# Kernel tuning notes

Hardware: AMD Instinct MI355X
Metric: run time of the kernel (lower is better)

Reference implementation:

```python
import jax, jax.numpy as jnp
import numpy as np

S, TM1, B, V, E, H = 96, 96, 8, 32000, 256, 512
PAD = 0
NEG = -1e30


def setup_inputs() -> dict:
    key = jax.random.key(0)
    ks = jax.random.split(key, 10)
    n = lambda k, shape, s=0.05: (jax.random.normal(k, shape, jnp.float32) * s)
    return {
        "src": jax.random.randint(ks[0], (S, B), 0, V, jnp.int32),
        "tgt": jax.random.randint(ks[1], (TM1 + 1, B), 0, V, jnp.int32),
        "emb": n(ks[2], (V, E)),
        "W_ih": n(ks[3], (4 * H, E)),
        "W_hh": n(ks[4], (4 * H, H)),
        "b_ih": jnp.zeros((4 * H,), jnp.float32),
        "b_hh": jnp.zeros((4 * H,), jnp.float32),
        "W_att": n(ks[5], (H, H)),
        "sent": n(ks[6], (H,)),
        "W_read": n(ks[7], (V, H)),
    }


def _lstm_cell(x, h, c, W_ih, W_hh, b_ih, b_hh):
    g = x @ W_ih.T + b_ih + h @ W_hh.T + b_hh
    i, f, gg, o = jnp.split(g, 4, axis=-1)
    c = jax.nn.sigmoid(f) * c + jax.nn.sigmoid(i) * jnp.tanh(gg)
    h = jax.nn.sigmoid(o) * jnp.tanh(c)
    return h, c


def _forward(src, tgt, emb, W_ih, W_hh, b_ih, b_hh, W_att, sent, W_read):
    # padding_idx behavior: pad row of embedding is zero (and gets no grad)
    emb_eff = emb * (jnp.arange(V) != PAD).astype(emb.dtype)[:, None]
    xs = jnp.concatenate([emb_eff[src], emb_eff[tgt[:-1]]], axis=0)  # [S+TM1,B,E]

    def step(carry, x):
        h, c = carry
        h, c = _lstm_cell(x, h, c, W_ih, W_hh, b_ih, b_hh)
        return (h, c), h

    init = (jnp.zeros((B, H), xs.dtype), jnp.zeros((B, H), xs.dtype))
    _, H_all = jax.lax.scan(step, init, xs)  # [S+TM1,B,H]

    H_dec = H_all[S:]                              # [TM1,B,H]
    Q = jnp.tanh(H_dec @ W_att.T)                  # [TM1,B,H]
    Z = jnp.einsum("tbh,jbh->tjb", Q, H_all)      # [TM1,S+TM1,B]
    zs = jnp.einsum("tbh,h->tb", Q, sent)         # sentinel logit
    logits = jnp.concatenate([Z, zs[:, None, :]], axis=1)  # [TM1,S+TM1+1,B]

    j = jnp.arange(S + TM1 + 1)
    t = jnp.arange(TM1)
    valid = (j[None, :] < S + t[:, None] + 1) | (j[None, :] == S + TM1)
    logits = jnp.where(valid[:, :, None], logits, NEG)
    a = jax.nn.softmax(logits, axis=1)
    a_src, a_tgt, a_sent = a[:, :S], a[:, S:S + TM1], a[:, -1]

    # pointer distributions via scatter-add (avoids dense one-hot [S,B,V])
    b_idx = jnp.arange(B)[None, None, :]
    t_idx = jnp.arange(TM1)[:, None, None]
    p_ptr = jnp.zeros((TM1, B, V), a.dtype)
    p_ptr = p_ptr.at[t_idx, b_idx, src[None, :, :]].add(a_src)
    p_ptr = p_ptr.at[t_idx, b_idx, tgt[:-1][None, :, :]].add(a_tgt)

    p_vocab = jax.nn.softmax(H_dec @ W_read.T, axis=-1)  # [TM1,B,V]
    p = p_ptr + p_vocab * a_sent[:, :, None]
    ptr_scores = p_ptr + a_sent[:, :, None]

    mask = (tgt != PAD).astype(p.dtype)  # [TM1+1,B]
    gold = jnp.take_along_axis(jnp.log(p), tgt[1:][:, :, None], axis=2)[..., 0] * mask[1:]
    gold_ptr = jnp.take_along_axis(jnp.log(ptr_scores), tgt[1:][:, :, None], axis=2)[..., 0] * mask[1:]
    return gold.sum(0), gold_ptr.sum(0)  # ([B], [B])


def reference(src, tgt, emb, W_ih, W_hh, b_ih, b_hh, W_att, sent, W_read):
    return _forward(src, tgt, emb, W_ih, W_hh, b_ih, b_hh, W_att, sent, W_read)
```

## Files before the change

### kernel.cpp

```cpp
#include <hip/hip_runtime.h>
#include <math.h>

#define SS   96
#define TM   96
#define BB   8
#define VV   32000
#define EE   256
#define HH   512
#define NTOK (SS + TM)
#define G4   (4 * HH)
#define NEGF (-1e30f)
#define LBLK 16
#define NVT  (VV / 64)

#define NXIH  768
#define NCVTW 512
#define NCVTR 8000
#define NPREP (NXIH + NCVTW + NCVTR)

typedef __attribute__((ext_vector_type(8))) short short8;
typedef __attribute__((ext_vector_type(4))) float f32x4;
typedef __attribute__((ext_vector_type(4))) unsigned uint32x4;
typedef unsigned long long u64;

#define XIH_OFF   ((size_t)0)
#define XIH_SZ    ((size_t)NTOK * BB * G4)
#define HALL_OFF  (XIH_OFF + XIH_SZ)
#define HALL_SZ   ((size_t)NTOK * BB * HH)
#define Q_OFF     (HALL_OFF + HALL_SZ)
#define Q_SZ      ((size_t)TM * BB * HH)
#define PPTR_OFF  (Q_OFF + Q_SZ)
#define ASENT_OFF (PPTR_OFF + (size_t)(TM * BB))
#define SSUM_OFF  (ASENT_OFF + (size_t)(TM * BB))
#define LSTAR_OFF (SSUM_OFF + (size_t)(TM * BB))
#define FLAG_OFF  (LSTAR_OFF + (size_t)(TM * BB))
#define HBF_OFF   (FLAG_OFF + (size_t)1024)
#define HBF_SZF   ((size_t)2 * BB * HH / 2)
#define WHHBF_OFF (HBF_OFF + HBF_SZF)
#define WHHBF_SZF ((size_t)G4 * HH / 2)
#define ABF_OFF   (WHHBF_OFF + WHHBF_SZF)
#define ABF_SZF   ((size_t)(TM * BB) * HH / 2)
#define WBF_OFF   (ABF_OFF + ABF_SZF)
#define WBF_SZF   ((size_t)VV * HH / 2)
#define PSUM_OFF  (WBF_OFF + WBF_SZF)
#define PSUM_SZF  ((size_t)NVT * (TM * BB))
#define NEED_F    (PSUM_OFF + PSUM_SZF)

__device__ __forceinline__ float sigf(float x) { return 1.f / (1.f + __expf(-x)); }

__device__ __forceinline__ unsigned short f2bf(float x) {
    unsigned bits = __float_as_uint(x);
    bits += 0x7FFFu + ((bits >> 16) & 1u);
    return (unsigned short)(bits >> 16);
}

__global__ void __launch_bounds__(256) k_prep(const int* __restrict__ src,
                                              const int* __restrict__ tgt,
                                              const float* __restrict__ emb,
                                              const float* __restrict__ Wih,
                                              const float* __restrict__ bih,
                                              const float* __restrict__ bhh,
                                              const float* __restrict__ Whh,
                                              const float* __restrict__ Wread,
                                              float* __restrict__ xih,
                                              unsigned short* __restrict__ whhbf,
                                              unsigned short* __restrict__ wbf) {
    __shared__ float xs[16 * EE];
    const int bid = blockIdx.x;
    const int tid = threadIdx.x;

    if (bid < NXIH) {
        const int tok0 = (bid >> 3) * 16;
        const int row0 = (bid & 7) * 256;
        for (int e = tid; e < 16 * EE; e += 256) {
            int tk = e >> 8, k = e & 255;
            int tau = tok0 + tk;
            int idx = (tau < SS * BB) ? src[tau] : tgt[tau - SS * BB];
            xs[tk * EE + k] = (idx == 0) ? 0.f : emb[(size_t)idx * EE + k];
        }
        __syncthreads();

        const int row = row0 + tid;
        const float bias = bih[row] + bhh[row];
        float acc[16];
#pragma unroll
        for (int r = 0; r < 16; ++r) acc[r] = bias;
        const float4* w4 = (const float4*)(Wih + (size_t)row * EE);
        for (int k4 = 0; k4 < EE / 4; ++k4) {
            float4 w = w4[k4];
#pragma unroll
            for (int r = 0; r < 16; ++r) {
                float4 x = *((const float4*)&xs[r * EE + k4 * 4]);
                acc[r] += w.x * x.x + w.y * x.y + w.z * x.z + w.w * x.w;
            }
        }
#pragma unroll
        for (int r = 0; r < 16; ++r)
            xih[(size_t)(tok0 + r) * G4 + row] = acc[r];
        return;
    }

    const float* srcp;
    unsigned short* dstp;
    size_t base;
    if (bid < NXIH + NCVTW) { srcp = Whh;   dstp = whhbf; base = (size_t)(bid - NXIH) * 2048; }
    else                    { srcp = Wread; dstp = wbf;   base = (size_t)(bid - NXIH - NCVTW) * 2048; }
    base += (size_t)tid * 8;
    float4 f0 = *(const float4*)(srcp + base);
    float4 f1 = *(const float4*)(srcp + base + 4);
    uint4 o;
    o.x = (unsigned)f2bf(f0.x) | ((unsigned)f2bf(f0.y) << 16);
    o.y = (unsigned)f2bf(f0.z) | ((unsigned)f2bf(f0.w) << 16);
    o.z = (unsigned)f2bf(f1.x) | ((unsigned)f2bf(f1.y) << 16);
    o.w = (unsigned)f2bf(f1.z) | ((unsigned)f2bf(f1.w) << 16);
    *(uint4*)(dstp + base) = o;
}

__global__ void __launch_bounds__(256, 1) k_lstm(const float* __restrict__ xih,
                                                 const unsigned short* __restrict__ whhbf,
                                                 float* __restrict__ hall,
                                                 unsigned short* __restrict__ hbf,
                                                 unsigned short* __restrict__ abf,
                                                 unsigned* __restrict__ flags) {
    __shared__ short lA[65536];
    const int tid = threadIdx.x;
    const int wv  = tid >> 6;
    const int l   = tid & 63;
    const int b16 = l & 15;
    const int kg  = l >> 4;
    const int bb  = b16 & 7;
    const int bx  = blockIdx.x;
    const int I0  = bx * 32 + wv * 8;

    const int j = b16;
    const unsigned short* a0p = whhbf + ((size_t)((j >> 3) * HH + I0 + (j & 7))) * HH + kg * 8;
    const unsigned short* a1p = whhbf + ((size_t)((2 + (j >> 3)) * HH + I0 + (j & 7))) * HH + kg * 8;
    short* lA0 = lA + (((size_t)wv * 2 + 0) * 16 * 64 + l) * 8;
    short* lA1 = lA + (((size_t)wv * 2 + 1) * 16 * 64 + l) * 8;
#pragma unroll
    for (int ks = 0; ks < 16; ++ks) {
        *(short8*)(lA0 + ks * 512) = *(const short8*)(a0p + ks * 32);
        *(short8*)(lA1 + ks * 512) = *(const short8*)(a1p + ks * 32);
    }
    __syncthreads();

    const int xgate0 = (kg >> 1);
    const int xgate1 = 2 + (kg >> 1);
    const int xi     = I0 + (kg & 1) * 4;

    float c0[4] = {0.f, 0.f, 0.f, 0.f};
    union fragu { uint32x4 u4; short8 s; };

    for (int t = 0; t < NTOK; ++t) {
        const float* xb = xih + ((size_t)t * BB + bb) * G4;
        float4 x0 = *(const float4*)(xb + xgate0 * HH + xi);
        float4 x1 = *(const float4*)(xb + xgate1 * HH + xi);

        fragu Bf[16];
        if (t > 0) {
            if (l < 16) {
                while (__hip_atomic_load(&flags[(size_t)l * 16], __ATOMIC_RELAXED,
                                         __HIP_MEMORY_SCOPE_AGENT) < (unsigned)t) {}
            }
            const unsigned short* hsrc =
                hbf + ((t - 1) & 1) * (BB * HH) + (size_t)bb * HH + kg * 8;
#pragma unroll
            for (int ks = 0; ks < 16; ++ks)
                asm volatile("global_load_dwordx4 %0, %1, off sc0 sc1"
                             : "=v"(Bf[ks].u4) : "v"(hsrc + ks * 32) : "memory");
            asm volatile("s_waitcnt vmcnt(0)" ::: "memory");
            __builtin_amdgcn_sched_barrier(0);
        }

        f32x4 acc0 = {x0.x, x0.y, x0.z, x0.w};
        f32x4 acc1 = {x1.x, x1.y, x1.z, x1.w};
        if (t > 0) {
#pragma unroll
            for (int ks = 0; ks < 16; ++ks) {
                short8 a0 = *(const short8*)(lA0 + ks * 512);
                short8 a1 = *(const short8*)(lA1 + ks * 512);
                acc0 = __builtin_amdgcn_mfma_f32_16x16x32_bf16(a0, Bf[ks].s, acc0, 0, 0, 0);
                acc1 = __builtin_amdgcn_mfma_f32_16x16x32_bf16(a1, Bf[ks].s, acc1, 0, 0, 0);
            }
        }

        float hreg[4];
#pragma unroll
        for (int r = 0; r < 4; ++r) {
            float gf = __shfl_down(acc0[r], 32, 64);
            float go = __shfl_down(acc1[r], 32, 64);
            float is = sigf(acc0[r]);
            float fs = sigf(gf);
            float gv = tanhf(acc1[r]);
            float os = sigf(go);
            c0[r] = fs * c0[r] + is * gv;
            hreg[r] = os * tanhf(c0[r]);
        }

        if (l < 32 && b16 < BB) {
            const int ib = I0 + kg * 4;
            *(float4*)(hall + ((size_t)t * BB + b16) * HH + ib) =
                make_float4(hreg[0], hreg[1], hreg[2], hreg[3]);
            u64 pk = (u64)f2bf(hreg[0]) | ((u64)f2bf(hreg[1]) << 16) |
                     ((u64)f2bf(hreg[2]) << 32) | ((u64)f2bf(hreg[3]) << 48);
            if (t >= SS)
                *(u64*)(abf + ((size_t)(t - SS) * BB + b16) * HH + ib) = pk;
            if (t < NTOK - 1) {
                unsigned short* hdst = hbf + (t & 1) * (BB * HH) + (size_t)b16 * HH + ib;
                asm volatile("global_store_dwordx2 %0, %1, off sc0 sc1"
                             :: "v"(hdst), "v"(pk) : "memory");
            }
        }

        if (t < NTOK - 1) {
            asm volatile("s_waitcnt vmcnt(0)" ::: "memory");
            __syncthreads();
            if (tid == 0)
                __hip_atomic_store(&flags[(size_t)bx * 16], (unsigned)(t + 1),
                                   __ATOMIC_RELAXED, __HIP_MEMORY_SCOPE_AGENT);
        }
    }
}

__global__ void __launch_bounds__(256) k_q(const float* __restrict__ hall,
                                           const float* __restrict__ Watt,
                                           float* __restrict__ q) {
    __shared__ float hb[8 * 516];
    const int t = blockIdx.x, tid = threadIdx.x;
    const float* hdec = hall + (size_t)(SS + t) * (BB * HH);
    for (int e = tid; e < BB * HH; e += 256)
        hb[(e >> 9) * 516 + (e & 511)] = hdec[e];
    __syncthreads();

    for (int oi = tid; oi < BB * HH; oi += 256) {
        int b = oi & 7, ii = oi >> 3;
        const float4* w4 = (const float4*)(Watt + (size_t)ii * HH);
        const float4* h4 = (const float4*)(hb + b * 516);
        float acc = 0.f;
        for (int k4 = 0; k4 < HH / 4; ++k4) {
            float4 w = w4[k4], h = h4[k4];
            acc += w.x * h.x + w.y * h.y + w.z * h.z + w.w * h.w;
        }
        q[(size_t)(t * BB + b) * HH + ii] = tanhf(acc);
    }
}

__global__ void __launch_bounds__(256) k_att(const float* __restrict__ hall,
                                             const float* __restrict__ q,
                                             const float* __restrict__ sent,
                                             const int* __restrict__ src,
                                             const int* __restrict__ tgt,
                                             float* __restrict__ pptr,
                                             float* __restrict__ asent) {
    __shared__ float qs[HH];
    __shared__ float av[256];
    __shared__ float red[256];
    const int t = blockIdx.x, b = blockIdx.y, tid = threadIdx.x;

    for (int e = tid; e < HH; e += 256) qs[e] = q[(size_t)(t * BB + b) * HH + e];
    __syncthreads();

    const int j = tid;
    float acc = NEGF;
    if (j < SS + TM + 1) {
        bool valid = (j < SS + t + 1) || (j == SS + TM);
        if (valid) {
            const float* vptr = (j < SS + TM) ? (hall + (size_t)(j * BB + b) * HH) : sent;
            const float4* v4 = (const float4*)vptr;
            const float4* q4 = (const float4*)qs;
            float a = 0.f;
            for (int k4 = 0; k4 < HH / 4; ++k4) {
                float4 v = v4[k4], qq = q4[k4];
                a += v.x * qq.x + v.y * qq.y + v.z * qq.z + v.w * qq.w;
            }
            acc = a;
        }
    }
    red[tid] = acc;
    __syncthreads();
    for (int s2 = 128; s2 > 0; s2 >>= 1) {
        if (tid < s2) red[tid] = fmaxf(red[tid], red[tid + s2]);
        __syncthreads();
    }
    float m = red[0];
    __syncthreads();
    float e = __expf(acc - m);
    red[tid] = e;
    __syncthreads();
    for (int s2 = 128; s2 > 0; s2 >>= 1) {
        if (tid < s2) red[tid] += red[tid + s2];
        __syncthreads();
    }
    float denom = red[0];
    __syncthreads();
    float a = e / denom;
    av[tid] = a;
    __syncthreads();

    const int vs = tgt[(t + 1) * BB + b];
    float contrib = 0.f;
    if (j < SS) {
        if (src[j * BB + b] == vs) contrib += av[j];
        if (tgt[j * BB + b] == vs) contrib += av[SS + j];
    }
    red[tid] = contrib;
    __syncthreads();
    for (int s2 = 128; s2 > 0; s2 >>= 1) {
        if (tid < s2) red[tid] += red[tid + s2];
        __syncthreads();
    }
    if (tid == 0) {
        pptr[t * BB + b]  = red[0];
        asent[t * BB + b] = av[SS + TM];
    }
}

__global__ void __launch_bounds__(256) k_vocab_mfma(const unsigned short* __restrict__ Abf,
                                                    const unsigned short* __restrict__ Wbf,
                                                    const int* __restrict__ tgt,
                                                    float* __restrict__ psum,
                                                    float* __restrict__ lstar) {
    __shared__ short lB[32768];
    const int tid  = threadIdx.x;
    const int lane = tid & 63;
    const int r16  = lane & 15;
    const int kg   = lane >> 4;
    const int n0   = blockIdx.x * 64;

    for (int s = tid; s < 4096; s += 256) {
        const int slot = s >> 6;
        const int cb = slot >> 4, ks = slot & 15;
        const int ll = s & 63;
        const int rr = ll & 15, kk = ll >> 4;
        *(short8*)(lB + (size_t)s * 8) =
            *(const short8*)(Wbf + (size_t)(n0 + cb * 16 + rr) * HH + ks * 32 + kk * 8);
    }
    __syncthreads();

    const short* lBme = lB + (size_t)lane * 8;

    for (int pass = 0; pass < 12; ++pass) {
        const int row0 = pass * 64 + (tid >> 6) * 16;
        const unsigned short* arow = Abf + (size_t)(row0 + r16) * HH + kg * 8;

        f32x4 acc0 = {0.f,0.f,0.f,0.f}, acc1 = acc0, acc2 = acc0, acc3 = acc0;
#pragma unroll
        for (int ks = 0; ks < 16; ++ks) {
            short8 a = *(const short8*)(arow + ks * 32);
            acc0 = __builtin_amdgcn_mfma_f32_16x16x32_bf16(a, *(const short8*)(lBme + (size_t)(0 * 16 + ks) * 512), acc0, 0, 0, 0);
            acc1 = __builtin_amdgcn_mfma_f32_16x16x32_bf16(a, *(const short8*)(lBme + (size_t)(1 * 16 + ks) * 512), acc1, 0, 0, 0);
            acc2 = __builtin_amdgcn_mfma_f32_16x16x32_bf16(a, *(const short8*)(lBme + (size_t)(2 * 16 + ks) * 512), acc2, 0, 0, 0);
            acc3 = __builtin_amdgcn_mfma_f32_16x16x32_bf16(a, *(const short8*)(lBme + (size_t)(3 * 16 + ks) * 512), acc3, 0, 0, 0);
        }

#pragma unroll
        for (int reg = 0; reg < 4; ++reg) {
            const int rowg = row0 + 4 * kg + reg;
            const int vs = tgt[BB + rowg];
            int cg;
            cg = n0 +  0 + r16; if (cg == vs) lstar[rowg] = acc0[reg];
            cg = n0 + 16 + r16; if (cg == vs) lstar[rowg] = acc1[reg];
            cg = n0 + 32 + r16; if (cg == vs) lstar[rowg] = acc2[reg];
            cg = n0 + 48 + r16; if (cg == vs) lstar[rowg] = acc3[reg];

            float v = __expf(acc0[reg]) + __expf(acc1[reg]) +
                      __expf(acc2[reg]) + __expf(acc3[reg]);
            v += __shfl_xor(v, 1, 64);
            v += __shfl_xor(v, 2, 64);
            v += __shfl_xor(v, 4, 64);
            v += __shfl_xor(v, 8, 64);
            if (r16 == 0) psum[(size_t)blockIdx.x * (TM * BB) + rowg] = v;
        }
    }
}

__global__ void __launch_bounds__(256) k_vocab_f32(const float* __restrict__ hall,
                                                   const float* __restrict__ Wread,
                                                   const int* __restrict__ tgt,
                                                   float* __restrict__ ssum,
                                                   float* __restrict__ lstar) {
    __shared__ float hs[32 * HH];
    const int tid = threadIdx.x;
    const int v0 = blockIdx.x * 512 + tid * 2;
    const int v1 = v0 + 1;
    const bool g0 = v0 < VV, g1 = v1 < VV;
    const float4* w40 = (const float4*)(Wread + (size_t)(g0 ? v0 : 0) * HH);
    const float4* w41 = (const float4*)(Wread + (size_t)(g1 ? v1 : 0) * HH);
    const int rbase0 = blockIdx.y * 128;

    for (int ch = 0; ch < 4; ++ch) {
        const int rbase = rbase0 + ch * 32;
        const float4* sp4 = (const float4*)(hall + ((size_t)SS * BB + rbase) * HH);
        float4* hs4 = (float4*)hs;
        for (int e = tid; e < 32 * HH / 4; e += 256) hs4[e] = sp4[e];
        __syncthreads();

        float acc0[32], acc1[32];
#pragma unroll
        for (int r = 0; r < 32; ++r) { acc0[r] = 0.f; acc1[r] = 0.f; }

        for (int k4 = 0; k4 < HH / 4; ++k4) {
            float4 w0 = w40[k4];
            float4 w1 = w41[k4];
#pragma unroll
            for (int r = 0; r < 32; ++r) {
                float4 h = *((const float4*)(hs + r * HH + k4 * 4));
                acc0[r] += w0.x * h.x + w0.y * h.y + w0.z * h.z + w0.w * h.w;
                acc1[r] += w1.x * h.x + w1.y * h.y + w1.z * h.z + w1.w * h.w;
            }
        }

#pragma unroll
        for (int r = 0; r < 32; ++r) {
            const int row = rbase + r;
            float val = 0.f;
            if (g0) val += __expf(acc0[r]);
            if (g1) val += __expf(acc1[r]);
#pragma unroll
            for (int d = 32; d > 0; d >>= 1) val += __shfl_xor(val, d, 64);
            if ((tid & 63) == 0) atomicAdd(&ssum[row], val);
            const int vs = tgt[row + BB];
            if (g0 && v0 == vs) lstar[row] = acc0[r];
            else if (g1 && v1 == vs) lstar[row] = acc1[r];
        }
        __syncthreads();
    }
}

__global__ void __launch_bounds__(768) k_final(const float* __restrict__ pptr,
                                               const float* __restrict__ asent,
                                               const float* __restrict__ ssum,
                                               const float* __restrict__ lstar,
                                               const float* __restrict__ psum,
                                               const int use_psum,
                                               const int* __restrict__ tgt,
                                               float* __restrict__ out) {
    __shared__ float g[TM * BB], gp[TM * BB];
    const int tid = threadIdx.x;
    float ss;
    if (use_psum) {
        float s0 = 0.f, s1 = 0.f, s2 = 0.f, s3 = 0.f;
        for (int q = 0; q < NVT; q += 4) {
            s0 += psum[(size_t)(q + 0) * (TM * BB) + tid];
            s1 += psum[(size_t)(q + 1) * (TM * BB) + tid];
            s2 += psum[(size_t)(q + 2) * (TM * BB) + tid];
            s3 += psum[(size_t)(q + 3) * (TM * BB) + tid];
        }
        ss = (s0 + s1) + (s2 + s3);
    } else {
        ss = ssum[tid];
    }

    const int vs = tgt[tid + BB];
    const float pv = __expf(lstar[tid]) / ss;
    const float ps = pptr[tid];
    const float as = asent[tid];
    if (vs != 0) {
        g[tid]  = logf(ps + pv * as);
        gp[tid] = logf(ps + as);
    } else {
        g[tid] = 0.f; gp[tid] = 0.f;
    }
    __syncthreads();
    if (tid < BB) {
        float su1 = 0.f, su2 = 0.f;
        for (int t = 0; t < TM; ++t) { su1 += g[t * BB + tid]; su2 += gp[t * BB + tid]; }
        out[tid] = su1;
        out[BB + tid] = su2;
    }
}

extern "C" void kernel_launch(void* const* d_in, const int* in_sizes, int n_in,
                              void* d_out, int out_size, void* d_ws, size_t ws_size,
                              hipStream_t stream) {
    (void)in_sizes; (void)n_in; (void)out_size;
    const int*   src   = (const int*)d_in[0];
    const int*   tgt   = (const int*)d_in[1];
    const float* emb   = (const float*)d_in[2];
    const float* Wih   = (const float*)d_in[3];
    const float* Whh   = (const float*)d_in[4];
    const float* bih   = (const float*)d_in[5];
    const float* bhh   = (const float*)d_in[6];
    const float* Watt  = (const float*)d_in[7];
    const float* sent  = (const float*)d_in[8];
    const float* Wread = (const float*)d_in[9];
    float* ws  = (float*)d_ws;
    float* out = (float*)d_out;

    const bool use_mfma_vocab = ws_size >= NEED_F * sizeof(float);

    (void)hipMemsetAsync((void*)(ws + SSUM_OFF), 0, (size_t)2560 * sizeof(float), stream);

    k_prep<<<dim3(NPREP), 256, 0, stream>>>(
        src, tgt, emb, Wih, bih, bhh, Whh, Wread,
        ws + XIH_OFF, (unsigned short*)(ws + WHHBF_OFF), (unsigned short*)(ws + WBF_OFF));

    k_lstm<<<dim3(LBLK), 256, 0, stream>>>(
        ws + XIH_OFF, (const unsigned short*)(ws + WHHBF_OFF), ws + HALL_OFF,
        (unsigned short*)(ws + HBF_OFF), (unsigned short*)(ws + ABF_OFF),
        (unsigned*)(ws + FLAG_OFF));

    k_q<<<dim3(TM), 256, 0, stream>>>(ws + HALL_OFF, Watt, ws + Q_OFF);

    k_att<<<dim3(TM, BB), 256, 0, stream>>>(ws + HALL_OFF, ws + Q_OFF, sent,
                                            src, tgt, ws + PPTR_OFF, ws + ASENT_OFF);

    if (use_mfma_vocab) {
        k_vocab_mfma<<<dim3(NVT), 256, 0, stream>>>(
            (const unsigned short*)(ws + ABF_OFF),
            (const unsigned short*)(ws + WBF_OFF),
            tgt, ws + PSUM_OFF, ws + LSTAR_OFF);
    } else {
        k_vocab_f32<<<dim3(63, 6), 256, 0, stream>>>(ws + HALL_OFF, Wread, tgt,
                                                     ws + SSUM_OFF, ws + LSTAR_OFF);
    }

    k_final<<<dim3(1), dim3(TM * BB), 0, stream>>>(ws + PPTR_OFF, ws + ASENT_OFF,
                                                   ws + SSUM_OFF, ws + LSTAR_OFF,
                                                   ws + PSUM_OFF, use_mfma_vocab ? 1 : 0,
                                                   tgt, out);
}
```

Baseline: 1.237 ms.

## Fuse bf16 weight conversion into consumers and merge attention with vocab kernel

```diff
diff --git a/kernel.cpp b/kernel.cpp
--- a/kernel.cpp
+++ b/kernel.cpp
@@ -12,11 +12,7 @@
 #define NEGF (-1e30f)
 #define LBLK 16
 #define NVT  (VV / 64)
-
-#define NXIH  768
-#define NCVTW 512
-#define NCVTR 8000
-#define NPREP (NXIH + NCVTW + NCVTR)
+#define NXIH 768
 
 typedef __attribute__((ext_vector_type(8))) short short8;
 typedef __attribute__((ext_vector_type(4))) float f32x4;
@@ -36,13 +32,9 @@
 #define FLAG_OFF  (LSTAR_OFF + (size_t)(TM * BB))
 #define HBF_OFF   (FLAG_OFF + (size_t)1024)
 #define HBF_SZF   ((size_t)2 * BB * HH / 2)
-#define WHHBF_OFF (HBF_OFF + HBF_SZF)
-#define WHHBF_SZF ((size_t)G4 * HH / 2)
-#define ABF_OFF   (WHHBF_OFF + WHHBF_SZF)
+#define ABF_OFF   (HBF_OFF + HBF_SZF)
 #define ABF_SZF   ((size_t)(TM * BB) * HH / 2)
-#define WBF_OFF   (ABF_OFF + ABF_SZF)
-#define WBF_SZF   ((size_t)VV * HH / 2)
-#define PSUM_OFF  (WBF_OFF + WBF_SZF)
+#define PSUM_OFF  (ABF_OFF + ABF_SZF)
 #define PSUM_SZF  ((size_t)NVT * (TM * BB))
 #define NEED_F    (PSUM_OFF + PSUM_SZF)
 
@@ -52,6 +44,13 @@
     unsigned bits = __float_as_uint(x);
     bits += 0x7FFFu + ((bits >> 16) & 1u);
     return (unsigned short)(bits >> 16);
+}
+
+__device__ __forceinline__ short8 pack_bf8(float4 f0, float4 f1) {
+    union { unsigned short u[8]; short8 s; } r;
+    r.u[0] = f2bf(f0.x); r.u[1] = f2bf(f0.y); r.u[2] = f2bf(f0.z); r.u[3] = f2bf(f0.w);
+    r.u[4] = f2bf(f1.x); r.u[5] = f2bf(f1.y); r.u[6] = f2bf(f1.z); r.u[7] = f2bf(f1.w);
+    return r.s;
 }
 
 __global__ void __launch_bounds__(256) k_prep(const int* __restrict__ src,
@@ -60,64 +59,42 @@
                                               const float* __restrict__ Wih,
                                               const float* __restrict__ bih,
                                               const float* __restrict__ bhh,
-                                              const float* __restrict__ Whh,
-                                              const float* __restrict__ Wread,
-                                              float* __restrict__ xih,
-                                              unsigned short* __restrict__ whhbf,
-                                              unsigned short* __restrict__ wbf) {
+                                              float* __restrict__ xih) {
     __shared__ float xs[16 * EE];
     const int bid = blockIdx.x;
     const int tid = threadIdx.x;
 
-    if (bid < NXIH) {
-        const int tok0 = (bid >> 3) * 16;
-        const int row0 = (bid & 7) * 256;
-        for (int e = tid; e < 16 * EE; e += 256) {
-            int tk = e >> 8, k = e & 255;
-            int tau = tok0 + tk;
-            int idx = (tau < SS * BB) ? src[tau] : tgt[tau - SS * BB];
-            xs[tk * EE + k] = (idx == 0) ? 0.f : emb[(size_t)idx * EE + k];
-        }
-        __syncthreads();
-
-        const int row = row0 + tid;
-        const float bias = bih[row] + bhh[row];
-        float acc[16];
-#pragma unroll
-        for (int r = 0; r < 16; ++r) acc[r] = bias;
-        const float4* w4 = (const float4*)(Wih + (size_t)row * EE);
-        for (int k4 = 0; k4 < EE / 4; ++k4) {
-            float4 w = w4[k4];
-#pragma unroll
-            for (int r = 0; r < 16; ++r) {
-                float4 x = *((const float4*)&xs[r * EE + k4 * 4]);
-                acc[r] += w.x * x.x + w.y * x.y + w.z * x.z + w.w * x.w;
-            }
-        }
-#pragma unroll
-        for (int r = 0; r < 16; ++r)
-            xih[(size_t)(tok0 + r) * G4 + row] = acc[r];
-        return;
-    }
-
-    const float* srcp;
-    unsigned short* dstp;
-    size_t base;
-    if (bid < NXIH + NCVTW) { srcp = Whh;   dstp = whhbf; base = (size_t)(bid - NXIH) * 2048; }
-    else                    { srcp = Wread; dstp = wbf;   base = (size_t)(bid - NXIH - NCVTW) * 2048; }
-    base += (size_t)tid * 8;
-    float4 f0 = *(const float4*)(srcp + base);
-    float4 f1 = *(const float4*)(srcp + base + 4);
-    uint4 o;
-    o.x = (unsigned)f2bf(f0.x) | ((unsigned)f2bf(f0.y) << 16);
-    o.y = (unsigned)f2bf(f0.z) | ((unsigned)f2bf(f0.w) << 16);
-    o.z = (unsigned)f2bf(f1.x) | ((unsigned)f2bf(f1.y) << 16);
-    o.w = (unsigned)f2bf(f1.z) | ((unsigned)f2bf(f1.w) << 16);
-    *(uint4*)(dstp + base) = o;
+    const int tok0 = (bid >> 3) * 16;
+    const int row0 = (bid & 7) * 256;
+    for (int e = tid; e < 16 * EE; e += 256) {
+        int tk = e >> 8, k = e & 255;
+        int tau = tok0 + tk;
+        int idx = (tau < SS * BB) ? src[tau] : tgt[tau - SS * BB];
+        xs[tk * EE + k] = (idx == 0) ? 0.f : emb[(size_t)idx * EE + k];
+    }
+    __syncthreads();
+
+    const int row = row0 + tid;
+    const float bias = bih[row] + bhh[row];
+    float acc[16];
+#pragma unroll
+    for (int r = 0; r < 16; ++r) acc[r] = bias;
+    const float4* w4 = (const float4*)(Wih + (size_t)row * EE);
+    for (int k4 = 0; k4 < EE / 4; ++k4) {
+        float4 w = w4[k4];
+#pragma unroll
+        for (int r = 0; r < 16; ++r) {
+            float4 x = *((const float4*)&xs[r * EE + k4 * 4]);
+            acc[r] += w.x * x.x + w.y * x.y + w.z * x.z + w.w * x.w;
+        }
+    }
+#pragma unroll
+    for (int r = 0; r < 16; ++r)
+        xih[(size_t)(tok0 + r) * G4 + row] = acc[r];
 }
 
 __global__ void __launch_bounds__(256, 1) k_lstm(const float* __restrict__ xih,
-                                                 const unsigned short* __restrict__ whhbf,
+                                                 const float* __restrict__ Whh,
                                                  float* __restrict__ hall,
                                                  unsigned short* __restrict__ hbf,
                                                  unsigned short* __restrict__ abf,
@@ -133,14 +110,16 @@
     const int I0  = bx * 32 + wv * 8;
 
     const int j = b16;
-    const unsigned short* a0p = whhbf + ((size_t)((j >> 3) * HH + I0 + (j & 7))) * HH + kg * 8;
-    const unsigned short* a1p = whhbf + ((size_t)((2 + (j >> 3)) * HH + I0 + (j & 7))) * HH + kg * 8;
+    const float* a0f = Whh + ((size_t)((j >> 3) * HH + I0 + (j & 7))) * HH + kg * 8;
+    const float* a1f = Whh + ((size_t)((2 + (j >> 3)) * HH + I0 + (j & 7))) * HH + kg * 8;
     short* lA0 = lA + (((size_t)wv * 2 + 0) * 16 * 64 + l) * 8;
     short* lA1 = lA + (((size_t)wv * 2 + 1) * 16 * 64 + l) * 8;
 #pragma unroll
     for (int ks = 0; ks < 16; ++ks) {
-        *(short8*)(lA0 + ks * 512) = *(const short8*)(a0p + ks * 32);
-        *(short8*)(lA1 + ks * 512) = *(const short8*)(a1p + ks * 32);
+        *(short8*)(lA0 + ks * 512) =
+            pack_bf8(*(const float4*)(a0f + ks * 32), *(const float4*)(a0f + ks * 32 + 4));
+        *(short8*)(lA1 + ks * 512) =
+            pack_bf8(*(const float4*)(a1f + ks * 32), *(const float4*)(a1f + ks * 32 + 4));
     }
     __syncthreads();
 
@@ -245,18 +224,15 @@
     }
 }
 
-__global__ void __launch_bounds__(256) k_att(const float* __restrict__ hall,
-                                             const float* __restrict__ q,
-                                             const float* __restrict__ sent,
-                                             const int* __restrict__ src,
-                                             const int* __restrict__ tgt,
-                                             float* __restrict__ pptr,
-                                             float* __restrict__ asent) {
-    __shared__ float qs[HH];
-    __shared__ float av[256];
-    __shared__ float red[256];
-    const int t = blockIdx.x, b = blockIdx.y, tid = threadIdx.x;
-
+__device__ __forceinline__ void att_body(int t, int b, int tid,
+                                         const float* __restrict__ hall,
+                                         const float* __restrict__ q,
+                                         const float* __restrict__ sent,
+                                         const int* __restrict__ src,
+                                         const int* __restrict__ tgt,
+                                         float* __restrict__ pptr,
+                                         float* __restrict__ asent,
+                                         float* qs, float* av, float* red) {
     for (int e = tid; e < HH; e += 256) qs[e] = q[(size_t)(t * BB + b) * HH + e];
     __syncthreads();
 
@@ -315,25 +291,58 @@
     }
 }
 
-__global__ void __launch_bounds__(256) k_vocab_mfma(const unsigned short* __restrict__ Abf,
-                                                    const unsigned short* __restrict__ Wbf,
-                                                    const int* __restrict__ tgt,
-                                                    float* __restrict__ psum,
-                                                    float* __restrict__ lstar) {
-    __shared__ short lB[32768];
-    const int tid  = threadIdx.x;
+__global__ void __launch_bounds__(256) k_att(const float* __restrict__ hall,
+                                             const float* __restrict__ q,
+                                             const float* __restrict__ sent,
+                                             const int* __restrict__ src,
+                                             const int* __restrict__ tgt,
+                                             float* __restrict__ pptr,
+                                             float* __restrict__ asent) {
+    __shared__ float qs[HH];
+    __shared__ float av[256];
+    __shared__ float red[256];
+    att_body(blockIdx.x, blockIdx.y, threadIdx.x, hall, q, sent, src, tgt,
+             pptr, asent, qs, av, red);
+}
+
+__global__ void __launch_bounds__(256) k_post(const unsigned short* __restrict__ Abf,
+                                              const float* __restrict__ Wread,
+                                              const float* __restrict__ hall,
+                                              const float* __restrict__ q,
+                                              const float* __restrict__ sent,
+                                              const int* __restrict__ src,
+                                              const int* __restrict__ tgt,
+                                              float* __restrict__ psum,
+                                              float* __restrict__ lstar,
+                                              float* __restrict__ pptr,
+                                              float* __restrict__ asent) {
+    __shared__ char smem[65536];
+    const int bid = blockIdx.x;
+    const int tid = threadIdx.x;
+
+    if (bid >= NVT) {
+        const int idx = bid - NVT;
+        float* qs  = (float*)smem;
+        float* av  = qs + HH;
+        float* red = av + 256;
+        att_body(idx >> 3, idx & 7, tid, hall, q, sent, src, tgt, pptr, asent, qs, av, red);
+        return;
+    }
+
+    short* lB = (short*)smem;
     const int lane = tid & 63;
     const int r16  = lane & 15;
     const int kg   = lane >> 4;
-    const int n0   = blockIdx.x * 64;
+    const int n0   = bid * 64;
 
     for (int s = tid; s < 4096; s += 256) {
         const int slot = s >> 6;
         const int cb = slot >> 4, ks = slot & 15;
         const int ll = s & 63;
         const int rr = ll & 15, kk = ll >> 4;
+        const float* wsrc = Wread + (size_t)(n0 + cb * 16 + rr) * HH + ks * 32 + kk * 8;
         *(short8*)(lB + (size_t)s * 8) =
-            *(const short8*)(Wbf + (size_t)(n0 + cb * 16 + rr) * HH + ks * 32 + kk * 8);
+            pack_bf8(*(const float4*)wsrc, *(const float4*)(wsrc + 4));
     }
     __syncthreads();
 
@@ -369,7 +378,7 @@
             v += __shfl_xor(v, 2, 64);
             v += __shfl_xor(v, 4, 64);
             v += __shfl_xor(v, 8, 64);
-            if (r16 == 0) psum[(size_t)blockIdx.x * (TM * BB) + rowg] = v;
+            if (r16 == 0) psum[(size_t)bid * (TM * BB) + rowg] = v;
         }
     }
 }
@@ -487,36 +496,33 @@
     float* ws  = (float*)d_ws;
     float* out = (float*)d_out;
 
-    const bool use_mfma_vocab = ws_size >= NEED_F * sizeof(float);
+    const bool use_mfma = ws_size >= NEED_F * sizeof(float);
 
     (void)hipMemsetAsync((void*)(ws + SSUM_OFF), 0, (size_t)2560 * sizeof(float), stream);
 
-    k_prep<<<dim3(NPREP), 256, 0, stream>>>(
-        src, tgt, emb, Wih, bih, bhh, Whh, Wread,
-        ws + XIH_OFF, (unsigned short*)(ws + WHHBF_OFF), (unsigned short*)(ws + WBF_OFF));
+    k_prep<<<dim3(NXIH), 256, 0, stream>>>(src, tgt, emb, Wih, bih, bhh, ws + XIH_OFF);
 
     k_lstm<<<dim3(LBLK), 256, 0, stream>>>(
-        ws + XIH_OFF, (const unsigned short*)(ws + WHHBF_OFF), ws + HALL_OFF,
+        ws + XIH_OFF, Whh, ws + HALL_OFF,
         (unsigned short*)(ws + HBF_OFF), (unsigned short*)(ws + ABF_OFF),
         (unsigned*)(ws + FLAG_OFF));
 
     k_q<<<dim3(TM), 256, 0, stream>>>(ws + HALL_OFF, Watt, ws + Q_OFF);
 
-    k_att<<<dim3(TM, BB), 256, 0, stream>>>(ws + HALL_OFF, ws + Q_OFF, sent,
-                                            src, tgt, ws + PPTR_OFF, ws + ASENT_OFF);
-
-    if (use_mfma_vocab) {
-        k_vocab_mfma<<<dim3(NVT), 256, 0, stream>>>(
-            (const unsigned short*)(ws + ABF_OFF),
-            (const unsigned short*)(ws + WBF_OFF),
-            tgt, ws + PSUM_OFF, ws + LSTAR_OFF);
+    if (use_mfma) {
+        k_post<<<dim3(NVT + TM * BB), 256, 0, stream>>>(
+            (const unsigned short*)(ws + ABF_OFF), Wread,
+            ws + HALL_OFF, ws + Q_OFF, sent, src, tgt,
+            ws + PSUM_OFF, ws + LSTAR_OFF, ws + PPTR_OFF, ws + ASENT_OFF);
     } else {
+        k_att<<<dim3(TM, BB), 256, 0, stream>>>(ws + HALL_OFF, ws + Q_OFF, sent,
+                                                src, tgt, ws + PPTR_OFF, ws + ASENT_OFF);
         k_vocab_f32<<<dim3(63, 6), 256, 0, stream>>>(ws + HALL_OFF, Wread, tgt,
                                                      ws + SSUM_OFF, ws + LSTAR_OFF);
     }
 
     k_final<<<dim3(1), dim3(TM * BB), 0, stream>>>(ws + PPTR_OFF, ws + ASENT_OFF,
                                                    ws + SSUM_OFF, ws + LSTAR_OFF,
-                                                   ws + PSUM_OFF, use_mfma_vocab ? 1 : 0,
+                                                   ws + PSUM_OFF, use_mfma ? 1 : 0,
                                                    tgt, out);
 }
```

Result: no change. 1.260 ms (+1.9%).
